# Performance work log

Hardware: AMD Instinct MI355X
Metric: run time of the kernel (lower is better)

The kernel has to match this reference:

```python
import jax, jax.numpy as jnp
import numpy as np


def setup_inputs() -> dict:
    key = jax.random.key(0)
    k1, k2, k3, k4 = jax.random.split(key, 4)
    B, C, H, W = 8, 64, 64, 64
    Ck = C // 8  # query/key channels
    x = jax.random.normal(k1, (B, C, H, W), dtype=jnp.float32)
    # 1x1 conv1d weights (bias=False); spectral norm only rescales the weight,
    # so plain matrices are math-equivalent at a given parameter value.
    wq = jax.random.normal(k2, (Ck, C), dtype=jnp.float32) * (1.0 / np.sqrt(C))
    wk = jax.random.normal(k3, (Ck, C), dtype=jnp.float32) * (1.0 / np.sqrt(C))
    wv = jax.random.normal(k4, (C, C), dtype=jnp.float32) * (1.0 / np.sqrt(C))
    gamma = jnp.array([0.5], dtype=jnp.float32)  # nonzero so attention path is exercised
    return {"x": x, "wq": wq, "wk": wk, "wv": wv, "gamma": gamma}


def reference(x, wq, wk, wv, gamma):
    B, C, H, W = x.shape
    xf = x.reshape(B, C, H * W)                      # [B, C, N]
    f = jnp.einsum('kc,bcn->bkn', wq, xf)            # [B, C/8, N]
    g = jnp.einsum('kc,bcn->bkn', wk, xf)            # [B, C/8, N]
    h = jnp.einsum('oc,bcn->bon', wv, xf)            # [B, C,   N]
    scores = jnp.einsum('bkn,bkm->bnm', f, g)        # f^T g, [B, N, N]
    beta = jax.nn.softmax(scores, axis=1)            # softmax over dim=1 (rows), as in torch
    o = jnp.einsum('bcn,bnm->bcm', h, beta)          # [B, C, N]
    out = gamma[0] * o + xf
    return out.reshape(B, C, H, W)
```

## Files before the change

### kernel.cpp

```cpp
#include <hip/hip_runtime.h>
#include <hip/hip_bf16.h>

typedef __bf16 bf16x8 __attribute__((ext_vector_type(8)));
typedef float f32x4 __attribute__((ext_vector_type(4)));
typedef float f32x16 __attribute__((ext_vector_type(16)));
typedef unsigned int uint2v __attribute__((ext_vector_type(2)));

#define MFMA16 __builtin_amdgcn_mfma_f32_16x16x32_bf16
#define MFMA32 __builtin_amdgcn_mfma_f32_32x32x16_bf16

__device__ __forceinline__ unsigned short f2b(float f) {
  unsigned int u = __float_as_uint(f);
  u += 0x7FFFu + ((u >> 16) & 1u);
  return (unsigned short)(u >> 16);
}

__device__ __forceinline__ float b2f(unsigned short s) {
  return __uint_as_float(((unsigned)s) << 16);
}

union U128 {
  uint4 u;
  unsigned short s[8];
  bf16x8 b;
};

union BPack {
  __hip_bfloat162 h2;
  unsigned u;
};

__device__ __forceinline__ unsigned packbf(float a, float b) {
  BPack p;
  p.h2 = __float22bfloat162_rn(make_float2(a, b));
  return p.u;
}

__global__ __launch_bounds__(256, 2) void proj_kernel(
    const float* __restrict__ x, const float* __restrict__ wq,
    const float* __restrict__ wk, const float* __restrict__ wv_w,
    unsigned short* __restrict__ f_t, unsigned short* __restrict__ g_t,
    unsigned short* __restrict__ h_out) {
  __shared__ unsigned short xT[64 * 64];
  __shared__ unsigned short wT[96 * 72];
  __shared__ unsigned short hT[64 * 72];

  const int tid = (int)threadIdx.x;
  const int wvp = tid >> 6;
  const int lane = tid & 63;
  const int b = (int)blockIdx.x & 7;
  const int n0 = ((int)blockIdx.x >> 3) << 6;

  {
    const float* xb = x + ((size_t)b << 18) + n0 + lane;
    const int c0 = wvp * 16;
    float xv[16];
#pragma unroll
    for (int cc = 0; cc < 16; ++cc) xv[cc] = xb[(size_t)(c0 + cc) << 12];
#pragma unroll
    for (int p = 0; p < 4; ++p) {
      const int c = c0 + 4 * p;
      uint2 d;
      d.x = packbf(xv[4 * p + 0], xv[4 * p + 1]);
      d.y = packbf(xv[4 * p + 2], xv[4 * p + 3]);
      const int g = c >> 3;
      const int idx = lane * 64 + (((g ^ (lane & 7)) << 3) | (((c >> 2) & 1) << 2));
      *(uint2*)&xT[idx] = d;
    }
  }
#pragma unroll
  for (int i = 0; i < 20; ++i) {
    const int idx = i * 256 + tid;
    const float wval = (idx < 512) ? wq[idx] * 1.44269504f
                     : (idx < 1024) ? wk[idx - 512]
                                    : wv_w[idx - 1024];
    wT[(idx >> 6) * 72 + (idx & 63)] = f2b(wval);
  }
  __syncthreads();

  const int t = lane & 15, q = lane >> 4;
  const int nloc = wvp * 16 + t;
  U128 Bf[2];
#pragma unroll
  for (int kp = 0; kp < 2; ++kp) {
    const int g = kp * 4 + q;
    Bf[kp].u = *(const uint4*)&xT[nloc * 64 + ((g ^ (nloc & 7)) << 3)];
  }
  const int nabs = n0 + nloc;

  {
    f32x4 acc = {0.f, 0.f, 0.f, 0.f};
#pragma unroll
    for (int kp = 0; kp < 2; ++kp) {
      U128 Af;
      Af.u = *(const uint4*)&wT[t * 72 + ((kp * 4 + q) << 3)];
      acc = MFMA16(Af.b, Bf[kp].b, acc, 0, 0, 0);
    }
    uint2 d;
    d.x = packbf(acc[0], acc[1]);
    d.y = packbf(acc[2], acc[3]);
    unsigned short* dst = (q & 2) ? g_t : f_t;
    *(uint2*)&dst[((size_t)((b << 12) + nabs) << 3) + ((q & 1) << 2)] = d;
  }
#pragma unroll
  for (int rt = 1; rt < 5; ++rt) {
    f32x4 acc = {0.f, 0.f, 0.f, 0.f};
#pragma unroll
    for (int kp = 0; kp < 2; ++kp) {
      U128 Af;
      Af.u = *(const uint4*)&wT[(rt * 16 + t) * 72 + ((kp * 4 + q) << 3)];
      acc = MFMA16(Af.b, Bf[kp].b, acc, 0, 0, 0);
    }
    const int cbase = (rt - 1) * 16 + 4 * q;
#pragma unroll
    for (int reg = 0; reg < 4; ++reg)
      hT[(cbase + reg) * 72 + nloc] = f2b(acc[reg]);
  }
  __syncthreads();

  {
    const int hc = tid & 63;
    const int hw = tid >> 6;
    const uint4 v0 = *(const uint4*)&hT[hc * 72 + hw * 16];
    const uint4 v1 = *(const uint4*)&hT[hc * 72 + hw * 16 + 8];
    const size_t hbase =
        ((size_t)b << 18) + ((size_t)((n0 + hw * 16) >> 3) << 9) + (hc << 3);
    *(uint4*)&h_out[hbase] = v0;
    *(uint4*)&h_out[hbase + 512] = v1;
  }
}

__global__ __launch_bounds__(256, 2) void attn_kernel(
    const unsigned short* __restrict__ f_t, const unsigned short* __restrict__ g_t,
    const unsigned short* __restrict__ h, const float* __restrict__ x,
    const float* __restrict__ gamma, float* __restrict__ out) {
  __shared__ unsigned short Opart[4][16][66];
  __shared__ float lred[4][64];
  __shared__ float lsum[64];

  const int tid = (int)threadIdx.x;
  const int wave = tid >> 6;
  const int lane = tid & 63;
  const int ml = lane & 31;
  const int hh = lane >> 5;

  const int b = (int)blockIdx.x & 7;
  const int m0 = ((int)blockIdx.x >> 3) << 6;

  const unsigned short* fb = f_t + ((size_t)b << 15);
  const unsigned short* hb = h + ((size_t)b << 18);

  U128 G0, G1;
  G0.u = make_uint4(0u, 0u, 0u, 0u);
  G1.u = make_uint4(0u, 0u, 0u, 0u);
  if (hh == 0) {
    G0.u = *(const uint4*)(g_t + ((size_t)((b << 12) + m0 + ml) << 3));
    G1.u = *(const uint4*)(g_t + ((size_t)((b << 12) + m0 + 32 + ml) << 3));
  }

  f32x16 O00 = {}, O01 = {}, O10 = {}, O11 = {};
  float2 lp0v = make_float2(0.f, 0.f), lp1v = make_float2(0.f, 0.f);
  const f32x16 ZC = {};

  const int nbase = wave << 10;

  const unsigned short* fp = fb + ((size_t)(nbase + ml) << 3);
  const unsigned short* hp = hb + ((nbase >> 3) << 9) + (hh << 9) + (ml << 3);

  U128 F0, F1, Ha_e[4], Ha_o[4];
  f32x16 S0, S1;

  F0.u = *(const uint4*)(fp);
  F1.u = *(const uint4*)(fp + 256);
  Ha_e[0].u = *(const uint4*)(hp);
  Ha_e[1].u = *(const uint4*)(hp + 256);
  Ha_e[2].u = *(const uint4*)(hp + 1024);
  Ha_e[3].u = *(const uint4*)(hp + 1280);
  __builtin_amdgcn_s_setprio(1);
  S0 = MFMA32(F0.b, G0.b, ZC, 0, 0, 0);
  S1 = MFMA32(F0.b, G1.b, ZC, 0, 0, 0);
  __builtin_amdgcn_s_setprio(0);

  auto half = [&](f32x16& S, const U128& G, float2& lp, f32x16& Oa, f32x16& Ob,
                  const U128* Hv, const U128& Fn, bool produce) {
    float e[16];
#pragma unroll
    for (int r = 0; r < 16; ++r) e[r] = __builtin_amdgcn_exp2f(S[r]);
    if (produce) {
      __builtin_amdgcn_s_setprio(1);
      S = MFMA32(Fn.b, G.b, ZC, 0, 0, 0);
      __builtin_amdgcn_s_setprio(0);
    }
    lp.x += ((e[0] + e[2]) + (e[4] + e[6])) + ((e[8] + e[10]) + (e[12] + e[14]));
    lp.y += ((e[1] + e[3]) + (e[5] + e[7])) + ((e[9] + e[11]) + (e[13] + e[15]));
#pragma unroll
    for (int kt = 0; kt < 2; ++kt) {
      const unsigned A0 = packbf(e[8 * kt + 0], e[8 * kt + 1]);
      const unsigned A1 = packbf(e[8 * kt + 2], e[8 * kt + 3]);
      const unsigned B0 = packbf(e[8 * kt + 4], e[8 * kt + 5]);
      const unsigned B1 = packbf(e[8 * kt + 6], e[8 * kt + 7]);
      const uint2v r0 = __builtin_amdgcn_permlane32_swap(A0, B0, false, false);
      const uint2v r1 = __builtin_amdgcn_permlane32_swap(A1, B1, false, false);
      U128 P;
      P.u.x = r0[0];
      P.u.y = r1[0];
      P.u.z = r0[1];
      P.u.w = r1[1];
      __builtin_amdgcn_s_setprio(1);
      Oa = MFMA32(Hv[2 * kt + 0].b, P.b, Oa, 0, 0, 0);
      Ob = MFMA32(Hv[2 * kt + 1].b, P.b, Ob, 0, 0, 0);
      __builtin_amdgcn_s_setprio(0);
    }
  };
  auto body = [&](const U128* Hv, const U128& Fn, bool produce) {
    half(S0, G0, lp0v, O00, O01, Hv, Fn, produce);
    half(S1, G1, lp1v, O10, O11, Hv, Fn, produce);
  };

#pragma unroll 1
  for (int j = 0; j < 15; ++j) {
    Ha_o[0].u = *(const uint4*)(hp + 2048);
    Ha_o[1].u = *(const uint4*)(hp + 2304);
    Ha_o[2].u = *(const uint4*)(hp + 3072);
    Ha_o[3].u = *(const uint4*)(hp + 3328);
    F0.u = *(const uint4*)(fp + 512);
    body(Ha_e, F1, true);
    hp += 4096;
    Ha_e[0].u = *(const uint4*)(hp);
    Ha_e[1].u = *(const uint4*)(hp + 256);
    Ha_e[2].u = *(const uint4*)(hp + 1024);
    Ha_e[3].u = *(const uint4*)(hp + 1280);
    F1.u = *(const uint4*)(fp + 768);
    body(Ha_o, F0, true);
    fp += 512;
  }
  Ha_o[0].u = *(const uint4*)(hp + 2048);
  Ha_o[1].u = *(const uint4*)(hp + 2304);
  Ha_o[2].u = *(const uint4*)(hp + 3072);
  Ha_o[3].u = *(const uint4*)(hp + 3328);
  body(Ha_e, F1, true);
  body(Ha_o, F1, false);

  float lp0 = lp0v.x + lp0v.y;
  float lp1 = lp1v.x + lp1v.y;
  lp0 += __shfl_xor(lp0, 32, 64);
  lp1 += __shfl_xor(lp1, 32, 64);
  if (hh == 0) {
    lred[wave][ml] = lp0;
    lred[wave][32 + ml] = lp1;
  }

  const float gam = gamma[0];

  auto stash = [&](int p, const f32x16& Oa, const f32x16& Ob) {
    if ((ml >> 4) == (p & 1)) {
      const int mi = ml & 15;
#pragma unroll
      for (int r = 0; r < 8; ++r) {
        const int c0 = ((2 * r) & 3) + 8 * (r >> 1) + 4 * hh;
        *(unsigned*)&Opart[wave][mi][c0] = packbf(Oa[2 * r], Oa[2 * r + 1]);
        *(unsigned*)&Opart[wave][mi][c0 + 32] = packbf(Ob[2 * r], Ob[2 * r + 1]);
      }
    }
  };
  auto drain = [&](int p) {
    const int c = tid >> 2;
    const int m4 = (tid & 3) << 2;
    float a0 = 0.f, a1 = 0.f, a2 = 0.f, a3 = 0.f;
#pragma unroll
    for (int w = 0; w < 4; ++w) {
      a0 += b2f(Opart[w][m4 + 0][c]);
      a1 += b2f(Opart[w][m4 + 1][c]);
      a2 += b2f(Opart[w][m4 + 2][c]);
      a3 += b2f(Opart[w][m4 + 3][c]);
    }
    const f32x4 l = *(const f32x4*)&lsum[p * 16 + m4];
    const size_t oi = (((size_t)b * 64 + c) << 12) + m0 + p * 16 + m4;
    f32x4 xo = *(const f32x4*)(x + oi);
    xo[0] += gam / l[0] * a0;
    xo[1] += gam / l[1] * a1;
    xo[2] += gam / l[2] * a2;
    xo[3] += gam / l[3] * a3;
    *(f32x4*)(out + oi) = xo;
  };

  stash(0, O00, O01);
  __syncthreads();
  if (tid < 64)
    lsum[tid] = (lred[0][tid] + lred[1][tid]) + (lred[2][tid] + lred[3][tid]);
  __syncthreads();
  drain(0);
  __syncthreads();
  stash(1, O00, O01);
  __syncthreads();
  drain(1);
  __syncthreads();
  stash(2, O10, O11);
  __syncthreads();
  drain(2);
  __syncthreads();
  stash(3, O10, O11);
  __syncthreads();
  drain(3);
}

extern "C" void kernel_launch(void* const* d_in, const int* in_sizes, int n_in,
                              void* d_out, int out_size, void* d_ws, size_t ws_size,
                              hipStream_t stream) {
  (void)in_sizes; (void)n_in; (void)out_size; (void)ws_size;
  const float* x = (const float*)d_in[0];
  const float* wq = (const float*)d_in[1];
  const float* wk = (const float*)d_in[2];
  const float* wv = (const float*)d_in[3];
  const float* gamma = (const float*)d_in[4];
  float* out = (float*)d_out;

  unsigned short* f_t = (unsigned short*)d_ws;
  unsigned short* g_t = f_t + (size_t)8 * 4096 * 8;
  unsigned short* h = g_t + (size_t)8 * 4096 * 8;

  proj_kernel<<<512, 256, 0, stream>>>(x, wq, wk, wv, f_t, g_t, h);
  attn_kernel<<<512, 256, 0, stream>>>(f_t, g_t, h, x, gamma, out);
}
```

Baseline: 102.3 us.

## Triple-buffer H/F register prefetch and halve epilogue stash/drain rounds

The attention main loop moves from a two-stage (even/odd) register prefetch of H and F tiles to a three-stage rotation, so loads are issued two bodies ahead to hide global memory latency. The epilogue doubles the shared Opart buffer so each stash writes all 32 rows at once, cutting the stash/drain phases from four to two and removing several barriers. The trade-off is extra VGPR pressure from the third set of buffers, which could hurt occupancy at launch_bounds(256,2), plus more LDS use.

Result: slower. 126.7 us (+23.9%).

```diff
diff --git a/kernel.cpp b/kernel.cpp
--- a/kernel.cpp
+++ b/kernel.cpp
@@ -134,7 +134,7 @@
     const unsigned short* __restrict__ f_t, const unsigned short* __restrict__ g_t,
     const unsigned short* __restrict__ h, const float* __restrict__ x,
     const float* __restrict__ gamma, float* __restrict__ out) {
-  __shared__ unsigned short Opart[4][16][66];
+  __shared__ unsigned short Opart[4][32][66];
   __shared__ float lred[4][64];
   __shared__ float lsum[64];
 
@@ -167,18 +167,25 @@
   const unsigned short* fp = fb + ((size_t)(nbase + ml) << 3);
   const unsigned short* hp = hb + ((nbase >> 3) << 9) + (hh << 9) + (ml << 3);
 
-  U128 F0, F1, Ha_e[4], Ha_o[4];
+  U128 F_A, F_B, F_C, HaA[4], HaB[4], HaC[4];
   f32x16 S0, S1;
 
-  F0.u = *(const uint4*)(fp);
-  F1.u = *(const uint4*)(fp + 256);
-  Ha_e[0].u = *(const uint4*)(hp);
-  Ha_e[1].u = *(const uint4*)(hp + 256);
-  Ha_e[2].u = *(const uint4*)(hp + 1024);
-  Ha_e[3].u = *(const uint4*)(hp + 1280);
+  auto loadH = [&](U128* Hs, const unsigned short* base) {
+    Hs[0].u = *(const uint4*)(base);
+    Hs[1].u = *(const uint4*)(base + 256);
+    Hs[2].u = *(const uint4*)(base + 1024);
+    Hs[3].u = *(const uint4*)(base + 1280);
+  };
+
+  loadH(HaA, hp);
+  loadH(HaB, hp + 2048);
+  loadH(HaC, hp + 4096);
+  F_A.u = *(const uint4*)(fp);
+  F_B.u = *(const uint4*)(fp + 256);
+  F_C.u = *(const uint4*)(fp + 512);
   __builtin_amdgcn_s_setprio(1);
-  S0 = MFMA32(F0.b, G0.b, ZC, 0, 0, 0);
-  S1 = MFMA32(F0.b, G1.b, ZC, 0, 0, 0);
+  S0 = MFMA32(F_A.b, G0.b, ZC, 0, 0, 0);
+  S1 = MFMA32(F_A.b, G1.b, ZC, 0, 0, 0);
   __builtin_amdgcn_s_setprio(0);
 
   auto half = [&](f32x16& S, const U128& G, float2& lp, f32x16& Oa, f32x16& Ob,
@@ -218,28 +225,34 @@
   };
 
 #pragma unroll 1
-  for (int j = 0; j < 15; ++j) {
-    Ha_o[0].u = *(const uint4*)(hp + 2048);
-    Ha_o[1].u = *(const uint4*)(hp + 2304);
-    Ha_o[2].u = *(const uint4*)(hp + 3072);
-    Ha_o[3].u = *(const uint4*)(hp + 3328);
-    F0.u = *(const uint4*)(fp + 512);
-    body(Ha_e, F1, true);
-    hp += 4096;
-    Ha_e[0].u = *(const uint4*)(hp);
-    Ha_e[1].u = *(const uint4*)(hp + 256);
-    Ha_e[2].u = *(const uint4*)(hp + 1024);
-    Ha_e[3].u = *(const uint4*)(hp + 1280);
-    F1.u = *(const uint4*)(fp + 768);
-    body(Ha_o, F0, true);
-    fp += 512;
-  }
-  Ha_o[0].u = *(const uint4*)(hp + 2048);
-  Ha_o[1].u = *(const uint4*)(hp + 2304);
-  Ha_o[2].u = *(const uint4*)(hp + 3072);
-  Ha_o[3].u = *(const uint4*)(hp + 3328);
-  body(Ha_e, F1, true);
-  body(Ha_o, F1, false);
+  for (int j = 0; j < 9; ++j) {
+    body(HaA, F_B, true);
+    loadH(HaA, hp + 6144);
+    F_A.u = *(const uint4*)(fp + 768);
+    hp += 2048;
+    fp += 256;
+    body(HaB, F_C, true);
+    loadH(HaB, hp + 6144);
+    F_B.u = *(const uint4*)(fp + 768);
+    hp += 2048;
+    fp += 256;
+    body(HaC, F_A, true);
+    loadH(HaC, hp + 6144);
+    F_C.u = *(const uint4*)(fp + 768);
+    hp += 2048;
+    fp += 256;
+  }
+  body(HaA, F_B, true);
+  loadH(HaA, hp + 6144);
+  F_A.u = *(const uint4*)(fp + 768);
+  hp += 2048;
+  fp += 256;
+  body(HaB, F_C, true);
+  loadH(HaB, hp + 6144);
+  F_B.u = *(const uint4*)(fp + 768);
+  body(HaC, F_A, true);
+  body(HaA, F_B, true);
+  body(HaB, F_B, false);
 
   float lp0 = lp0v.x + lp0v.y;
   float lp1 = lp1v.x + lp1v.y;
@@ -252,56 +265,48 @@
 
   const float gam = gamma[0];
 
-  auto stash = [&](int p, const f32x16& Oa, const f32x16& Ob) {
-    if ((ml >> 4) == (p & 1)) {
-      const int mi = ml & 15;
-#pragma unroll
-      for (int r = 0; r < 8; ++r) {
-        const int c0 = ((2 * r) & 3) + 8 * (r >> 1) + 4 * hh;
-        *(unsigned*)&Opart[wave][mi][c0] = packbf(Oa[2 * r], Oa[2 * r + 1]);
-        *(unsigned*)&Opart[wave][mi][c0 + 32] = packbf(Ob[2 * r], Ob[2 * r + 1]);
-      }
+  auto stash = [&](const f32x16& Oa, const f32x16& Ob) {
+#pragma unroll
+    for (int r = 0; r < 8; ++r) {
+      const int c0 = ((2 * r) & 3) + 8 * (r >> 1) + 4 * hh;
+      *(unsigned*)&Opart[wave][ml][c0] = packbf(Oa[2 * r], Oa[2 * r + 1]);
+      *(unsigned*)&Opart[wave][ml][c0 + 32] = packbf(Ob[2 * r], Ob[2 * r + 1]);
     }
   };
   auto drain = [&](int p) {
     const int c = tid >> 2;
-    const int m4 = (tid & 3) << 2;
-    float a0 = 0.f, a1 = 0.f, a2 = 0.f, a3 = 0.f;
-#pragma unroll
-    for (int w = 0; w < 4; ++w) {
-      a0 += b2f(Opart[w][m4 + 0][c]);
-      a1 += b2f(Opart[w][m4 + 1][c]);
-      a2 += b2f(Opart[w][m4 + 2][c]);
-      a3 += b2f(Opart[w][m4 + 3][c]);
-    }
-    const f32x4 l = *(const f32x4*)&lsum[p * 16 + m4];
-    const size_t oi = (((size_t)b * 64 + c) << 12) + m0 + p * 16 + m4;
-    f32x4 xo = *(const f32x4*)(x + oi);
-    xo[0] += gam / l[0] * a0;
-    xo[1] += gam / l[1] * a1;
-    xo[2] += gam / l[2] * a2;
-    xo[3] += gam / l[3] * a3;
-    *(f32x4*)(out + oi) = xo;
-  };
-
-  stash(0, O00, O01);
+    const int m8 = (tid & 3) << 3;
+    float a[8];
+#pragma unroll
+    for (int j = 0; j < 8; ++j) a[j] = 0.f;
+#pragma unroll
+    for (int w = 0; w < 4; ++w)
+#pragma unroll
+      for (int j = 0; j < 8; ++j) a[j] += b2f(Opart[w][m8 + j][c]);
+    const f32x4 l0 = *(const f32x4*)&lsum[p * 32 + m8];
+    const f32x4 l1 = *(const f32x4*)&lsum[p * 32 + m8 + 4];
+    const size_t oi = (((size_t)b * 64 + c) << 12) + m0 + p * 32 + m8;
+    f32x4 xo0 = *(const f32x4*)(x + oi);
+    f32x4 xo1 = *(const f32x4*)(x + oi + 4);
+#pragma unroll
+    for (int j = 0; j < 4; ++j) {
+      xo0[j] += gam / l0[j] * a[j];
+      xo1[j] += gam / l1[j] * a[j + 4];
+    }
+    *(f32x4*)(out + oi) = xo0;
+    *(f32x4*)(out + oi + 4) = xo1;
+  };
+
+  stash(O00, O01);
   __syncthreads();
   if (tid < 64)
     lsum[tid] = (lred[0][tid] + lred[1][tid]) + (lred[2][tid] + lred[3][tid]);
   __syncthreads();
   drain(0);
   __syncthreads();
-  stash(1, O00, O01);
+  stash(O10, O11);
   __syncthreads();
   drain(1);
-  __syncthreads();
-  stash(2, O10, O11);
-  __syncthreads();
-  drain(2);
-  __syncthreads();
-  stash(3, O10, O11);
-  __syncthreads();
-  drain(3);
 }
 
 extern "C" void kernel_launch(void* const* d_in, const int* in_sizes, int n_in,
```
